# Kernel tuning notes

Measured on AMD Instinct MI355X. Metric: run time of the kernel, lower is better.

The kernel has to match this reference:

```python
import jax, jax.numpy as jnp
import numpy as np

B, S, E, O = 8, 4096, 512, 512
DT, STEPS = 0.01, 10


def setup_inputs() -> dict:
    key = jax.random.key(0)
    ks = jax.random.split(key, 8)
    sc = 1.0 / np.sqrt(E)
    return {
        "x": jax.random.normal(ks[0], (B, S, E), jnp.float32),
        "W1": jax.random.normal(ks[1], (E, O), jnp.float32) * sc,
        "b1": jnp.zeros((O,), jnp.float32),
        "W2": jax.random.normal(ks[2], (O, O), jnp.float32) * sc,
        "b2": jnp.zeros((O,), jnp.float32),
        "omega": jax.random.normal(ks[3], (O,), jnp.float32) * 0.1,
        "K": jnp.float32(1.0),
        "alpha": jnp.float32(0.1),
        "F1": jax.random.normal(ks[4], (O, E), jnp.float32) * sc,
        "c1": jnp.zeros((E,), jnp.float32),
        "F2": jax.random.normal(ks[5], (E, E), jnp.float32) * sc,
        "c2": jnp.zeros((E,), jnp.float32),
        "noise": jax.random.normal(ks[6], (B, S, E), jnp.float32),
    }


def reference(x, W1, b1, W2, b2, omega, K, alpha, F1, c1, F2, c2, noise):
    # phase_sync: Linear -> Tanh -> Linear, applied per token
    phases = jnp.tanh(jnp.einsum("bse,eo->bso", x, W1) + b1)
    phases = jnp.einsum("bso,op->bsp", phases, W2) + b2  # [B,S,O]

    # 10-step Kuramoto recurrence
    def step(ph, _):
        mean_field = jnp.mean(jnp.sin(ph), axis=-1, keepdims=True)  # [B,S,1]
        dph = omega + K * mean_field * jnp.cos(ph)
        return ph + DT * dph, None

    phases, _ = jax.lax.scan(step, phases, None, length=STEPS)

    # fractal_layer: Linear -> ReLU -> Linear
    h = jax.nn.relu(jnp.einsum("bso,oe->bse", phases, F1) + c1)
    consciousness = jnp.einsum("bse,ef->bsf", h, F2) + c2  # [B,S,E]

    fractal_mod = jnp.sin(alpha * jnp.arange(E, dtype=jnp.float32))  # [E]
    # noise broadcast to 3 imaginary channels, modulated along embed dim
    imag = noise[..., None] * fractal_mod[None, None, :, None]  # [B,S,E,1]
    imag = jnp.broadcast_to(imag, consciousness.shape + (3,))
    return jnp.concatenate([consciousness[..., None], imag], axis=-1)  # [B,S,E,4]
```

## Files before the change

kernel.cpp:

```cpp
#include <hip/hip_runtime.h>
#include <math.h>

#define MTOT 32768
#define KDIM 512
#define NDIM 512

typedef __attribute__((ext_vector_type(8))) short short8;
typedef __attribute__((ext_vector_type(4))) float f32x4;
typedef __attribute__((ext_vector_type(4))) unsigned int uint4v;

__device__ __forceinline__ unsigned short f2b(float f) {
  unsigned int u = __builtin_bit_cast(unsigned int, f);
  u = (u + 0x7fffu + ((u >> 16) & 1u)) >> 16;
  return (unsigned short)u;
}
__device__ __forceinline__ float b2f(unsigned short h) {
  unsigned int u = ((unsigned int)h) << 16;
  return __builtin_bit_cast(float, u);
}

__device__ __forceinline__ float fast_tanh(float x) {
  float e = __expf(2.0f * x);
  return 1.0f - 2.0f / (e + 1.0f);
}

__device__ __forceinline__ void async_copy16(const unsigned short* g, unsigned short* l) {
  __builtin_amdgcn_global_load_lds(
      (const __attribute__((address_space(1))) unsigned int*)g,
      (__attribute__((address_space(3))) unsigned int*)l, 16, 0, 0);
}

__global__ __launch_bounds__(256)
void xcast_k(const float* __restrict__ x, unsigned short* __restrict__ out) {
  const size_t i = ((size_t)blockIdx.x * 256 + threadIdx.x) * 8;
  f32x4 a = *(const f32x4*)(x + i);
  f32x4 b = *(const f32x4*)(x + i + 4);
  unsigned short t[8] __attribute__((aligned(16)));
  t[0]=f2b(a[0]); t[1]=f2b(a[1]); t[2]=f2b(a[2]); t[3]=f2b(a[3]);
  t[4]=f2b(b[0]); t[5]=f2b(b[1]); t[6]=f2b(b[2]); t[7]=f2b(b[3]);
  *(uint4v*)(out + i) = *(const uint4v*)t;
}

__global__ __launch_bounds__(256)
void transpose_w4(const float* __restrict__ i0, const float* __restrict__ i1,
                  const float* __restrict__ i2, const float* __restrict__ i3,
                  unsigned short* __restrict__ o0, unsigned short* __restrict__ o1,
                  unsigned short* __restrict__ o2, unsigned short* __restrict__ o3) {
  const float* in;
  unsigned short* out;
  switch (blockIdx.z) {
    case 0: in = i0; out = o0; break;
    case 1: in = i1; out = o1; break;
    case 2: in = i2; out = o2; break;
    default: in = i3; out = o3; break;
  }
  __shared__ float t[32][33];
  const int tx = threadIdx.x, ty = threadIdx.y;
  const int n0 = blockIdx.x * 32, k0 = blockIdx.y * 32;
  #pragma unroll
  for (int i = 0; i < 32; i += 8)
    t[ty + i][tx] = in[(size_t)(k0 + ty + i) * NDIM + (n0 + tx)];
  __syncthreads();
  #pragma unroll
  for (int i = 0; i < 32; i += 8)
    out[(size_t)(n0 + ty + i) * KDIM + (k0 + tx)] = f2b(t[tx][ty + i]);
}

template<int ACT>
__global__ __launch_bounds__(256, 2)
void gemm_k(const unsigned short* __restrict__ A,
            const unsigned short* __restrict__ Bt,
            const float* __restrict__ bias,
            unsigned short* __restrict__ Cout,
            const float* __restrict__ noise,
            const float* __restrict__ alphap,
            float* __restrict__ Out4)
{
  __shared__ __align__(16) unsigned short As[128][64];
  __shared__ __align__(16) unsigned short Bs[128][64];

  const int tid  = threadIdx.x;
  const int wave = tid >> 6, lane = tid & 63;
  const int quad = lane >> 4, l16 = lane & 15;
  const int wm = (wave >> 1) * 64, wn = (wave & 1) * 64;

  const int id  = blockIdx.x;
  const int xcd = id & 7;
  const int s   = id >> 3;
  const int bn  = (s & 3) * 128;
  const int bm  = ((s >> 2) * 8 + xcd) * 128;

  const int r8 = lane >> 3;
  const int lc = (lane & 7) ^ r8;
  const unsigned short* aSrc = A  + (size_t)(bm + wave*32 + r8) * KDIM + lc*8;
  const unsigned short* bSrc = Bt + (size_t)(bn + wave*32 + r8) * KDIM + lc*8;

  f32x4 acc[4][4] = {};

  for (int k0 = 0; k0 < KDIM; k0 += 64) {
    #pragma unroll
    for (int j = 0; j < 4; j++) {
      async_copy16(aSrc + j*8*KDIM + k0, &As[wave*32 + j*8][0]);
      async_copy16(bSrc + j*8*KDIM + k0, &Bs[wave*32 + j*8][0]);
    }
    __syncthreads();

    #pragma unroll
    for (int kc = 0; kc < 2; kc++) {
      const int ca = (((kc*4 + quad) ^ (l16 & 7)) * 8);
      short8 af[4], bfr[4];
      #pragma unroll
      for (int mi = 0; mi < 4; mi++)
        af[mi] = *(const short8*)&As[wm + mi*16 + l16][ca];
      #pragma unroll
      for (int ni = 0; ni < 4; ni++)
        bfr[ni] = *(const short8*)&Bs[wn + ni*16 + l16][ca];
      __builtin_amdgcn_s_setprio(1);
      #pragma unroll
      for (int mi = 0; mi < 4; mi++)
        #pragma unroll
        for (int ni = 0; ni < 4; ni++)
          acc[mi][ni] = __builtin_amdgcn_mfma_f32_16x16x32_bf16(
              af[mi], bfr[ni], acc[mi][ni], 0, 0, 0);
      __builtin_amdgcn_s_setprio(0);
    }
    __syncthreads();
  }

  float bias_v[4];
  #pragma unroll
  for (int ni = 0; ni < 4; ni++) bias_v[ni] = bias[bn + wn + ni*16 + l16];

  if (ACT == 3) {
    const float alpha = alphap[0];
    float fmod[4];
    #pragma unroll
    for (int ni = 0; ni < 4; ni++)
      fmod[ni] = sinf(alpha * (float)(bn + wn + ni*16 + l16));
    #pragma unroll
    for (int mi = 0; mi < 4; mi++) {
      #pragma unroll
      for (int ni = 0; ni < 4; ni++) {
        const int n = bn + wn + ni*16 + l16;
        #pragma unroll
        for (int r = 0; r < 4; r++) {
          const int m = bm + wm + mi*16 + quad*4 + r;
          const float c  = acc[mi][ni][r] + bias_v[ni];
          const float im = noise[(size_t)m * NDIM + n] * fmod[ni];
          f32x4 o; o[0] = c; o[1] = im; o[2] = im; o[3] = im;
          *(f32x4*)&Out4[((size_t)m * NDIM + n) * 4] = o;
        }
      }
    }
  } else {
    #pragma unroll
    for (int mi = 0; mi < 4; mi++) {
      #pragma unroll
      for (int ni = 0; ni < 4; ni++) {
        const int n = bn + wn + ni*16 + l16;
        #pragma unroll
        for (int r = 0; r < 4; r++) {
          const int m = bm + wm + mi*16 + quad*4 + r;
          float c = acc[mi][ni][r] + bias_v[ni];
          if (ACT == 0) c = fast_tanh(c);
          if (ACT == 2) c = fmaxf(c, 0.0f);
          Cout[(size_t)m * NDIM + n] = f2b(c);
        }
      }
    }
  }
}

__global__ __launch_bounds__(256)
void kuramoto_k(unsigned short* __restrict__ P,
                const float* __restrict__ omega,
                const float* __restrict__ Kp)
{
  const int lane  = threadIdx.x & 63;
  const int token = blockIdx.x * 4 + (threadIdx.x >> 6);
  const size_t base = (size_t)token * 512;
  const float Ks = Kp[0] * (1.0f / 512.0f);

  float ph[8], om[8];
  #pragma unroll
  for (int i = 0; i < 8; i++) {
    ph[i] = b2f(P[base + i*64 + lane]);
    om[i] = omega[i*64 + lane];
  }
  #pragma unroll
  for (int s = 0; s < 10; s++) {
    float sum = 0.0f;
    #pragma unroll
    for (int i = 0; i < 8; i++) sum += __sinf(ph[i]);
    #pragma unroll
    for (int off = 32; off > 0; off >>= 1) sum += __shfl_xor(sum, off, 64);
    const float mf = Ks * sum;
    #pragma unroll
    for (int i = 0; i < 8; i++) ph[i] += 0.01f * (om[i] + mf * __cosf(ph[i]));
  }
  #pragma unroll
  for (int i = 0; i < 8; i++) P[base + i*64 + lane] = f2b(ph[i]);
}

extern "C" void kernel_launch(void* const* d_in, const int* in_sizes, int n_in,
                              void* d_out, int out_size, void* d_ws, size_t ws_size,
                              hipStream_t stream) {
  const float* x      = (const float*)d_in[0];
  const float* W1     = (const float*)d_in[1];
  const float* b1     = (const float*)d_in[2];
  const float* W2     = (const float*)d_in[3];
  const float* b2     = (const float*)d_in[4];
  const float* omega  = (const float*)d_in[5];
  const float* Kp     = (const float*)d_in[6];
  const float* alphap = (const float*)d_in[7];
  const float* F1     = (const float*)d_in[8];
  const float* c1     = (const float*)d_in[9];
  const float* F2     = (const float*)d_in[10];
  const float* c2     = (const float*)d_in[11];
  const float* noise  = (const float*)d_in[12];
  float* out = (float*)d_out;

  char* ws = (char*)d_ws;
  unsigned short* wt1  = (unsigned short*)(ws + 0 * (512 * 1024));
  unsigned short* wt2  = (unsigned short*)(ws + 1 * (512 * 1024));
  unsigned short* wt3  = (unsigned short*)(ws + 2 * (512 * 1024));
  unsigned short* wt4  = (unsigned short*)(ws + 3 * (512 * 1024));
  unsigned short* xb   = (unsigned short*)(ws + 4 * (512 * 1024));
  unsigned short* bufA = xb   + (size_t)MTOT * 512;
  unsigned short* bufB = bufA + (size_t)MTOT * 512;

  dim3 tb(32, 8), tg(16, 16, 4);
  transpose_w4<<<tg, tb, 0, stream>>>(W1, W2, F1, F2, wt1, wt2, wt3, wt4);
  xcast_k<<<(MTOT * KDIM) / (256 * 8), 256, 0, stream>>>(x, xb);

  const int gg = 1024;
  gemm_k<0><<<gg, 256, 0, stream>>>(xb,   wt1, b1, bufA, nullptr, nullptr, nullptr);
  gemm_k<1><<<gg, 256, 0, stream>>>(bufA, wt2, b2, bufB, nullptr, nullptr, nullptr);
  kuramoto_k<<<MTOT / 4, 256, 0, stream>>>(bufB, omega, Kp);
  gemm_k<2><<<gg, 256, 0, stream>>>(bufB, wt3, c1, bufA, nullptr, nullptr, nullptr);
  gemm_k<3><<<gg, 256, 0, stream>>>(bufA, wt4, c2, nullptr, noise, alphap, out);
}
```

Before: 498.6 us.

## Fuse cast, four GEMMs and Kuramoto into one row-block megakernel

Replaces the separate x-cast, four GEMM launches and the Kuramoto kernel with a single kernel. Each block owns 32 token rows and keeps the bf16 activations in a swizzled 32KB LDS tile across all stages, so intermediates are never written to or read from global memory. Weight fragments are now loaded straight from global/L2 per wave instead of being staged through LDS. With only 32 rows per block, each weight fetch is reused far less, which greatly increases L2 weight traffic. The stages inside a block also run one after another, so MFMA work and Kuramoto math cannot overlap.

```diff
diff --git a/kernel.cpp b/kernel.cpp
--- a/kernel.cpp
+++ b/kernel.cpp
@@ -2,8 +2,8 @@
 #include <math.h>
 
 #define MTOT 32768
-#define KDIM 512
-#define NDIM 512
+#define MT   32
+#define NBLK (MTOT / MT)
 
 typedef __attribute__((ext_vector_type(8))) short short8;
 typedef __attribute__((ext_vector_type(4))) float f32x4;
@@ -18,27 +18,9 @@
   unsigned int u = ((unsigned int)h) << 16;
   return __builtin_bit_cast(float, u);
 }
-
 __device__ __forceinline__ float fast_tanh(float x) {
   float e = __expf(2.0f * x);
   return 1.0f - 2.0f / (e + 1.0f);
-}
-
-__device__ __forceinline__ void async_copy16(const unsigned short* g, unsigned short* l) {
-  __builtin_amdgcn_global_load_lds(
-      (const __attribute__((address_space(1))) unsigned int*)g,
-      (__attribute__((address_space(3))) unsigned int*)l, 16, 0, 0);
-}
-
-__global__ __launch_bounds__(256)
-void xcast_k(const float* __restrict__ x, unsigned short* __restrict__ out) {
-  const size_t i = ((size_t)blockIdx.x * 256 + threadIdx.x) * 8;
-  f32x4 a = *(const f32x4*)(x + i);
-  f32x4 b = *(const f32x4*)(x + i + 4);
-  unsigned short t[8] __attribute__((aligned(16)));
-  t[0]=f2b(a[0]); t[1]=f2b(a[1]); t[2]=f2b(a[2]); t[3]=f2b(a[3]);
-  t[4]=f2b(b[0]); t[5]=f2b(b[1]); t[6]=f2b(b[2]); t[7]=f2b(b[3]);
-  *(uint4v*)(out + i) = *(const uint4v*)t;
 }
 
 __global__ __launch_bounds__(256)
@@ -59,147 +41,171 @@
   const int n0 = blockIdx.x * 32, k0 = blockIdx.y * 32;
   #pragma unroll
   for (int i = 0; i < 32; i += 8)
-    t[ty + i][tx] = in[(size_t)(k0 + ty + i) * NDIM + (n0 + tx)];
+    t[ty + i][tx] = in[(size_t)(k0 + ty + i) * 512 + (n0 + tx)];
   __syncthreads();
   #pragma unroll
   for (int i = 0; i < 32; i += 8)
-    out[(size_t)(n0 + ty + i) * KDIM + (k0 + tx)] = f2b(t[tx][ty + i]);
-}
-
-template<int ACT>
+    out[(size_t)(n0 + ty + i) * 512 + (k0 + tx)] = f2b(t[tx][ty + i]);
+}
+
+template<int SACT>
+__device__ __forceinline__ void do_stage(
+    unsigned short* act,
+    const unsigned short* __restrict__ wt,
+    const float* __restrict__ bias,
+    const int wave, const int lane, const int r0,
+    const float* __restrict__ noise,
+    const float* __restrict__ alphap,
+    float* __restrict__ out4)
+{
+  const int quad = lane >> 4, l16 = lane & 15;
+  const int bn = wave * 128;
+
+  const unsigned short* wp[8];
+  #pragma unroll
+  for (int ni = 0; ni < 8; ++ni)
+    wp[ni] = wt + (size_t)(bn + ni * 16 + l16) * 512 + quad * 8;
+
+  f32x4 acc[2][8] = {};
+
+  #pragma unroll 2
+  for (int kc = 0; kc < 16; ++kc) {
+    const int row0 = l16;
+    const int row1 = 16 + l16;
+    const int p0 = (4 * kc + quad) ^ (row0 & 7);
+    const int p1 = (4 * kc + quad) ^ (row1 & 7);
+    short8 af0 = *(const short8*)&act[row0 * 512 + p0 * 8];
+    short8 af1 = *(const short8*)&act[row1 * 512 + p1 * 8];
+    short8 bf[8];
+    #pragma unroll
+    for (int ni = 0; ni < 8; ++ni)
+      bf[ni] = *(const short8*)(wp[ni] + kc * 32);
+    __builtin_amdgcn_s_setprio(1);
+    #pragma unroll
+    for (int ni = 0; ni < 8; ++ni) {
+      acc[0][ni] = __builtin_amdgcn_mfma_f32_16x16x32_bf16(af0, bf[ni], acc[0][ni], 0, 0, 0);
+      acc[1][ni] = __builtin_amdgcn_mfma_f32_16x16x32_bf16(af1, bf[ni], acc[1][ni], 0, 0, 0);
+    }
+    __builtin_amdgcn_s_setprio(0);
+  }
+
+  float bv[8];
+  #pragma unroll
+  for (int ni = 0; ni < 8; ++ni) bv[ni] = bias[bn + ni * 16 + l16];
+
+  if (SACT == 3) {
+    const float alpha = alphap[0];
+    float fmod[8];
+    #pragma unroll
+    for (int ni = 0; ni < 8; ++ni)
+      fmod[ni] = sinf(alpha * (float)(bn + ni * 16 + l16));
+    #pragma unroll
+    for (int mi = 0; mi < 2; ++mi) {
+      #pragma unroll
+      for (int ni = 0; ni < 8; ++ni) {
+        const int n = bn + ni * 16 + l16;
+        #pragma unroll
+        for (int r = 0; r < 4; ++r) {
+          const int m = r0 + mi * 16 + quad * 4 + r;
+          const float c  = acc[mi][ni][r] + bv[ni];
+          const float im = noise[(size_t)m * 512 + n] * fmod[ni];
+          f32x4 o; o[0] = c; o[1] = im; o[2] = im; o[3] = im;
+          *(f32x4*)&out4[((size_t)m * 512 + n) * 4] = o;
+        }
+      }
+    }
+  } else {
+    __syncthreads();
+    #pragma unroll
+    for (int mi = 0; mi < 2; ++mi) {
+      #pragma unroll
+      for (int ni = 0; ni < 8; ++ni) {
+        const int col = bn + ni * 16 + l16;
+        #pragma unroll
+        for (int r = 0; r < 4; ++r) {
+          const int row = mi * 16 + quad * 4 + r;
+          float c = acc[mi][ni][r] + bv[ni];
+          if (SACT == 0) c = fast_tanh(c);
+          if (SACT == 2) c = fmaxf(c, 0.0f);
+          const int phys = (col >> 3) ^ (row & 7);
+          act[row * 512 + phys * 8 + (col & 7)] = f2b(c);
+        }
+      }
+    }
+    __syncthreads();
+  }
+}
+
 __global__ __launch_bounds__(256, 2)
-void gemm_k(const unsigned short* __restrict__ A,
-            const unsigned short* __restrict__ Bt,
-            const float* __restrict__ bias,
-            unsigned short* __restrict__ Cout,
-            const float* __restrict__ noise,
-            const float* __restrict__ alphap,
-            float* __restrict__ Out4)
+void mega_k(const float* __restrict__ x,
+            const unsigned short* __restrict__ wt1, const float* __restrict__ b1,
+            const unsigned short* __restrict__ wt2, const float* __restrict__ b2,
+            const unsigned short* __restrict__ wt3, const float* __restrict__ c1,
+            const unsigned short* __restrict__ wt4, const float* __restrict__ c2,
+            const float* __restrict__ omega, const float* __restrict__ Kp,
+            const float* __restrict__ alphap, const float* __restrict__ noise,
+            float* __restrict__ out)
 {
-  __shared__ __align__(16) unsigned short As[128][64];
-  __shared__ __align__(16) unsigned short Bs[128][64];
+  __shared__ __align__(16) unsigned short act[MT * 512];
 
   const int tid  = threadIdx.x;
   const int wave = tid >> 6, lane = tid & 63;
-  const int quad = lane >> 4, l16 = lane & 15;
-  const int wm = (wave >> 1) * 64, wn = (wave & 1) * 64;
-
-  const int id  = blockIdx.x;
-  const int xcd = id & 7;
-  const int s   = id >> 3;
-  const int bn  = (s & 3) * 128;
-  const int bm  = ((s >> 2) * 8 + xcd) * 128;
-
-  const int r8 = lane >> 3;
-  const int lc = (lane & 7) ^ r8;
-  const unsigned short* aSrc = A  + (size_t)(bm + wave*32 + r8) * KDIM + lc*8;
-  const unsigned short* bSrc = Bt + (size_t)(bn + wave*32 + r8) * KDIM + lc*8;
-
-  f32x4 acc[4][4] = {};
-
-  for (int k0 = 0; k0 < KDIM; k0 += 64) {
-    #pragma unroll
-    for (int j = 0; j < 4; j++) {
-      async_copy16(aSrc + j*8*KDIM + k0, &As[wave*32 + j*8][0]);
-      async_copy16(bSrc + j*8*KDIM + k0, &Bs[wave*32 + j*8][0]);
-    }
-    __syncthreads();
-
-    #pragma unroll
-    for (int kc = 0; kc < 2; kc++) {
-      const int ca = (((kc*4 + quad) ^ (l16 & 7)) * 8);
-      short8 af[4], bfr[4];
-      #pragma unroll
-      for (int mi = 0; mi < 4; mi++)
-        af[mi] = *(const short8*)&As[wm + mi*16 + l16][ca];
-      #pragma unroll
-      for (int ni = 0; ni < 4; ni++)
-        bfr[ni] = *(const short8*)&Bs[wn + ni*16 + l16][ca];
-      __builtin_amdgcn_s_setprio(1);
-      #pragma unroll
-      for (int mi = 0; mi < 4; mi++)
-        #pragma unroll
-        for (int ni = 0; ni < 4; ni++)
-          acc[mi][ni] = __builtin_amdgcn_mfma_f32_16x16x32_bf16(
-              af[mi], bfr[ni], acc[mi][ni], 0, 0, 0);
-      __builtin_amdgcn_s_setprio(0);
-    }
-    __syncthreads();
-  }
-
-  float bias_v[4];
-  #pragma unroll
-  for (int ni = 0; ni < 4; ni++) bias_v[ni] = bias[bn + wn + ni*16 + l16];
-
-  if (ACT == 3) {
-    const float alpha = alphap[0];
-    float fmod[4];
-    #pragma unroll
-    for (int ni = 0; ni < 4; ni++)
-      fmod[ni] = sinf(alpha * (float)(bn + wn + ni*16 + l16));
-    #pragma unroll
-    for (int mi = 0; mi < 4; mi++) {
-      #pragma unroll
-      for (int ni = 0; ni < 4; ni++) {
-        const int n = bn + wn + ni*16 + l16;
-        #pragma unroll
-        for (int r = 0; r < 4; r++) {
-          const int m = bm + wm + mi*16 + quad*4 + r;
-          const float c  = acc[mi][ni][r] + bias_v[ni];
-          const float im = noise[(size_t)m * NDIM + n] * fmod[ni];
-          f32x4 o; o[0] = c; o[1] = im; o[2] = im; o[3] = im;
-          *(f32x4*)&Out4[((size_t)m * NDIM + n) * 4] = o;
-        }
-      }
-    }
-  } else {
-    #pragma unroll
-    for (int mi = 0; mi < 4; mi++) {
-      #pragma unroll
-      for (int ni = 0; ni < 4; ni++) {
-        const int n = bn + wn + ni*16 + l16;
-        #pragma unroll
-        for (int r = 0; r < 4; r++) {
-          const int m = bm + wm + mi*16 + quad*4 + r;
-          float c = acc[mi][ni][r] + bias_v[ni];
-          if (ACT == 0) c = fast_tanh(c);
-          if (ACT == 2) c = fmaxf(c, 0.0f);
-          Cout[(size_t)m * NDIM + n] = f2b(c);
-        }
-      }
-    }
-  }
-}
-
-__global__ __launch_bounds__(256)
-void kuramoto_k(unsigned short* __restrict__ P,
-                const float* __restrict__ omega,
-                const float* __restrict__ Kp)
-{
-  const int lane  = threadIdx.x & 63;
-  const int token = blockIdx.x * 4 + (threadIdx.x >> 6);
-  const size_t base = (size_t)token * 512;
-  const float Ks = Kp[0] * (1.0f / 512.0f);
-
-  float ph[8], om[8];
-  #pragma unroll
-  for (int i = 0; i < 8; i++) {
-    ph[i] = b2f(P[base + i*64 + lane]);
-    om[i] = omega[i*64 + lane];
-  }
-  #pragma unroll
-  for (int s = 0; s < 10; s++) {
-    float sum = 0.0f;
-    #pragma unroll
-    for (int i = 0; i < 8; i++) sum += __sinf(ph[i]);
-    #pragma unroll
-    for (int off = 32; off > 0; off >>= 1) sum += __shfl_xor(sum, off, 64);
-    const float mf = Ks * sum;
-    #pragma unroll
-    for (int i = 0; i < 8; i++) ph[i] += 0.01f * (om[i] + mf * __cosf(ph[i]));
-  }
-  #pragma unroll
-  for (int i = 0; i < 8; i++) P[base + i*64 + lane] = f2b(ph[i]);
+  const int r0   = blockIdx.x * MT;
+
+  #pragma unroll
+  for (int j = 0; j < 8; ++j) {
+    const int r  = wave * 8 + j;
+    const int lc = lane ^ (r & 7);
+    const float* src = x + (size_t)(r0 + r) * 512 + lc * 8;
+    f32x4 a = *(const f32x4*)src;
+    f32x4 b = *(const f32x4*)(src + 4);
+    unsigned short t[8] __attribute__((aligned(16)));
+    t[0] = f2b(a[0]); t[1] = f2b(a[1]); t[2] = f2b(a[2]); t[3] = f2b(a[3]);
+    t[4] = f2b(b[0]); t[5] = f2b(b[1]); t[6] = f2b(b[2]); t[7] = f2b(b[3]);
+    *(uint4v*)&act[r * 512 + lane * 8] = *(const uint4v*)t;
+  }
+  __syncthreads();
+
+  do_stage<0>(act, wt1, b1, wave, lane, r0, nullptr, nullptr, nullptr);
+  do_stage<1>(act, wt2, b2, wave, lane, r0, nullptr, nullptr, nullptr);
+
+  {
+    const float Ks = Kp[0] * (1.0f / 512.0f);
+    float om[8];
+    #pragma unroll
+    for (int i = 0; i < 8; ++i) om[i] = omega[i * 64 + lane];
+    for (int j = 0; j < 8; ++j) {
+      const int r = wave * 8 + j;
+      float ph[8];
+      #pragma unroll
+      for (int i = 0; i < 8; ++i) {
+        const int col = i * 64 + lane;
+        const int phys = (col >> 3) ^ (r & 7);
+        ph[i] = b2f(act[r * 512 + phys * 8 + (col & 7)]);
+      }
+      #pragma unroll
+      for (int s = 0; s < 10; ++s) {
+        float sum = 0.0f;
+        #pragma unroll
+        for (int i = 0; i < 8; ++i) sum += __sinf(ph[i]);
+        #pragma unroll
+        for (int off = 32; off > 0; off >>= 1) sum += __shfl_xor(sum, off, 64);
+        const float mf = Ks * sum;
+        #pragma unroll
+        for (int i = 0; i < 8; ++i) ph[i] += 0.01f * (om[i] + mf * __cosf(ph[i]));
+      }
+      #pragma unroll
+      for (int i = 0; i < 8; ++i) {
+        const int col = i * 64 + lane;
+        const int phys = (col >> 3) ^ (r & 7);
+        act[r * 512 + phys * 8 + (col & 7)] = f2b(ph[i]);
+      }
+    }
+  }
+  __syncthreads();
+
+  do_stage<2>(act, wt3, c1, wave, lane, r0, nullptr, nullptr, nullptr);
+  do_stage<3>(act, wt4, c2, wave, lane, r0, noise, alphap, out);
 }
 
 extern "C" void kernel_launch(void* const* d_in, const int* in_sizes, int n_in,
@@ -221,22 +227,13 @@
   float* out = (float*)d_out;
 
   char* ws = (char*)d_ws;
-  unsigned short* wt1  = (unsigned short*)(ws + 0 * (512 * 1024));
-  unsigned short* wt2  = (unsigned short*)(ws + 1 * (512 * 1024));
-  unsigned short* wt3  = (unsigned short*)(ws + 2 * (512 * 1024));
-  unsigned short* wt4  = (unsigned short*)(ws + 3 * (512 * 1024));
-  unsigned short* xb   = (unsigned short*)(ws + 4 * (512 * 1024));
-  unsigned short* bufA = xb   + (size_t)MTOT * 512;
-  unsigned short* bufB = bufA + (size_t)MTOT * 512;
+  unsigned short* wt1 = (unsigned short*)(ws + 0 * (512 * 1024));
+  unsigned short* wt2 = (unsigned short*)(ws + 1 * (512 * 1024));
+  unsigned short* wt3 = (unsigned short*)(ws + 2 * (512 * 1024));
+  unsigned short* wt4 = (unsigned short*)(ws + 3 * (512 * 1024));
 
   dim3 tb(32, 8), tg(16, 16, 4);
   transpose_w4<<<tg, tb, 0, stream>>>(W1, W2, F1, F2, wt1, wt2, wt3, wt4);
-  xcast_k<<<(MTOT * KDIM) / (256 * 8), 256, 0, stream>>>(x, xb);
-
-  const int gg = 1024;
-  gemm_k<0><<<gg, 256, 0, stream>>>(xb,   wt1, b1, bufA, nullptr, nullptr, nullptr);
-  gemm_k<1><<<gg, 256, 0, stream>>>(bufA, wt2, b2, bufB, nullptr, nullptr, nullptr);
-  kuramoto_k<<<MTOT / 4, 256, 0, stream>>>(bufB, omega, Kp);
-  gemm_k<2><<<gg, 256, 0, stream>>>(bufB, wt3, c1, bufA, nullptr, nullptr, nullptr);
-  gemm_k<3><<<gg, 256, 0, stream>>>(bufA, wt4, c2, nullptr, noise, alphap, out);
-}
+  mega_k<<<NBLK, 256, 0, stream>>>(x, wt1, b1, wt2, b2, wt3, c1, wt4, c2,
+                                   omega, Kp, alphap, noise, out);
+}
```

Measured after the change: 621.0 us. 1.25x slower.
